# Optimization experiments

Hardware: AMD Instinct MI355X
Metric: run time of the kernel (lower is better)

## Reference

```python
import jax, jax.numpy as jnp
import numpy as np

B = 256
D = 2048          # in_channels (shared latent dim)
S = 8             # n_subjects
OUT = 1000        # sum of 7 Schaefer network head widths [150,148,132,136,76,122,236]


def setup_inputs() -> dict:
    key = jax.random.key(0)
    k1, k2, k3, k4 = jax.random.split(key, 4)
    x = jax.random.normal(k1, (B, D), dtype=jnp.float32)
    subject_ids = jax.random.randint(k2, (B,), 0, S, dtype=jnp.int64)
    scale = 1.0 / np.sqrt(D)  # matches normal_(0, 1/in_channels**0.5)
    # Concatenated per-head weights: equivalent to 7 heads of shapes
    # (S, D, n_k) concatenated along the output axis (n_k sums to OUT).
    W = jax.random.normal(k3, (S, D, OUT), dtype=jnp.float32) * scale
    b = jax.random.normal(k4, (S, OUT), dtype=jnp.float32) * scale
    return {"x": x, "subject_ids": subject_ids, "W": W, "b": b}


def reference(x, subject_ids, W, b):
    # Per-sample weight gather (B, D, OUT) followed by batched matmul,
    # exactly mirroring torch: w = weights[subject_ids]; einsum('bd,bdo->bo').
    w = W[subject_ids]                      # (B, D, OUT) gathered copy
    out = jnp.einsum('bd,bdo->bo', x, w)    # (B, OUT)
    out = out + b[subject_ids]              # per-subject bias
    return out
```

## Files before the change

### kernel.cpp

```cpp
#include <hip/hip_runtime.h>
#include <stdint.h>

#define Bn   256
#define Dn   2048
#define Sn   8
#define ON   1000

#define ROWS 64
#define OT   64
#define KC   256
#define NDC  (Dn / KC)
#define NCH  (KC / 32)
#define NIT  (KC / 32)
#define LDK  (KC + 8)

typedef short v8s __attribute__((ext_vector_type(8)));
typedef float v4f __attribute__((ext_vector_type(4)));

static __device__ __forceinline__ short f2bf(float f) {
    union { float f; uint32_t u; } v; v.f = f;
    uint32_t u = v.u;
    u += 0x7FFFu + ((u >> 16) & 1u);
    return (short)(u >> 16);
}

__global__ __launch_bounds__(256) void main_kernel(const float* __restrict__ x,
                                                   const int* __restrict__ sid,
                                                   const float* __restrict__ W,
                                                   float* __restrict__ part) {
    __shared__ unsigned short Ash[ROWS * LDK];
    __shared__ unsigned short Bsh[OT * LDK];
    __shared__ unsigned long long bmask[4];
    __shared__ int rows_l[ROWS];

    const int oc = blockIdx.x;
    const int dc = blockIdx.y;
    const int s  = blockIdx.z;
    const int o0 = oc * OT;
    const int d0 = dc * KC;
    const int t  = threadIdx.x;
    const int lane = t & 63;
    const int wave = t >> 6;

    const int mysid = sid[t];
    const bool match = (mysid == s);
    const unsigned long long m = __ballot(match);
    if (lane == 0) bmask[wave] = m;
    if (t < ROWS) rows_l[t] = -1;
    __syncthreads();
    if (match) {
        int pos = __popcll(m & ((1ull << lane) - 1ull));
        for (int w = 0; w < wave; ++w) pos += __popcll(bmask[w]);
        if (pos < ROWS) rows_l[pos] = t;
    }
    __syncthreads();

    const int arow = t >> 2;
    const int ag   = t & 3;
    const int xrow = rows_l[arow];
    const float* xp = (xrow >= 0) ? (x + (size_t)xrow * Dn + d0 + ag * 8) : x;
    const int aoff0 = arow * LDK + ag * 8;

    int og = o0 + lane; if (og > ON - 1) og = ON - 1;
    const float* wp = W + (size_t)s * Dn * ON + (size_t)(d0 + wave * 8) * ON + og;
    const int boff0 = lane * LDK + wave * 8;

    float4 fa[2][2];
    float  fb[2][8];
#pragma unroll
    for (int c = 0; c < 2; ++c) {
#pragma unroll
        for (int j = 0; j < 8; j++) fb[c][j] = wp[(size_t)(c * 32 + j) * ON];
        fa[c][0] = *(const float4*)(xp + c * 32);
        fa[c][1] = *(const float4*)(xp + c * 32 + 4);
    }

#pragma unroll
    for (int c = 0; c < NCH; ++c) {
        const int sl = c & 1;
        v8s av;
        av[0] = f2bf(fa[sl][0].x); av[1] = f2bf(fa[sl][0].y);
        av[2] = f2bf(fa[sl][0].z); av[3] = f2bf(fa[sl][0].w);
        av[4] = f2bf(fa[sl][1].x); av[5] = f2bf(fa[sl][1].y);
        av[6] = f2bf(fa[sl][1].z); av[7] = f2bf(fa[sl][1].w);
        *(v8s*)&Ash[aoff0 + c * 32] = av;

        v8s bv;
#pragma unroll
        for (int j = 0; j < 8; j++) bv[j] = f2bf(fb[sl][j]);
        *(v8s*)&Bsh[boff0 + c * 32] = bv;

        if (c + 2 < NCH) {
#pragma unroll
            for (int j = 0; j < 8; j++) fb[sl][j] = wp[(size_t)((c + 2) * 32 + j) * ON];
            fa[sl][0] = *(const float4*)(xp + (c + 2) * 32);
            fa[sl][1] = *(const float4*)(xp + (c + 2) * 32 + 4);
        }
    }

    __syncthreads();

    const int lo16 = lane & 15;
    const int quad = lane >> 4;
    const int ar   = wave * 16 + lo16;

    v4f acc[4];
#pragma unroll
    for (int i = 0; i < 4; i++) acc[i] = (v4f){0.f, 0.f, 0.f, 0.f};

#pragma unroll
    for (int it = 0; it < NIT; ++it) {
        const v8s af = *(const v8s*)&Ash[ar * LDK + it * 32 + quad * 8];
#pragma unroll
        for (int nt = 0; nt < 4; nt++) {
            const v8s bf = *(const v8s*)&Bsh[(nt * 16 + lo16) * LDK + it * 32 + quad * 8];
            acc[nt] = __builtin_amdgcn_mfma_f32_16x16x32_bf16(af, bf, acc[nt], 0, 0, 0);
        }
    }

    float* pp = part + (size_t)dc * Bn * ON;
    const int er0 = wave * 16 + quad * 4;
#pragma unroll
    for (int nt = 0; nt < 4; nt++) {
        const int o = o0 + nt * 16 + lo16;
        if (o < ON) {
#pragma unroll
            for (int r = 0; r < 4; r++) {
                const int bi = rows_l[er0 + r];
                if (bi >= 0) pp[(size_t)bi * ON + o] = acc[nt][r];
            }
        }
    }
}

__global__ __launch_bounds__(256) void reduce_kernel(const int* __restrict__ sid,
                                                     const float* __restrict__ bias,
                                                     const float* __restrict__ part,
                                                     float* __restrict__ out) {
    const int b = blockIdx.x;
    const int s = sid[b];
    const int o = threadIdx.x * 4;
    if (o < ON) {
        float4 v = *(const float4*)(bias + (size_t)s * ON + o);
#pragma unroll
        for (int d = 0; d < NDC; d++) {
            const float4 p = *(const float4*)(part + ((size_t)d * Bn + b) * ON + o);
            v.x += p.x; v.y += p.y; v.z += p.z; v.w += p.w;
        }
        *(float4*)(out + (size_t)b * ON + o) = v;
    }
}

extern "C" void kernel_launch(void* const* d_in, const int* in_sizes, int n_in,
                              void* d_out, int out_size, void* d_ws, size_t ws_size,
                              hipStream_t stream) {
    const float* x    = (const float*)d_in[0];
    const int*   sid  = (const int*)d_in[1];
    const float* W    = (const float*)d_in[2];
    const float* bias = (const float*)d_in[3];
    float*       out  = (float*)d_out;
    float*       part = (float*)d_ws;

    main_kernel<<<dim3(16, NDC, Sn), dim3(256), 0, stream>>>(x, sid, W, part);
    reduce_kernel<<<dim3(Bn), dim3(256), 0, stream>>>(sid, bias, part, out);
}
```

Measured before the change: 111.9 us.

## Fuse split-K partials and reduction into single kernel with double-buffered K loop

Drops the split-K grid and the separate reduce kernel. Each block now loops over the full D dimension with double-buffered LDS and register prefetch of the next chunks, and adds the bias directly when it writes the output. This removes the partial-sum traffic to workspace and the second launch. In exchange the grid shrinks to 256 blocks with launch_bounds(256,1) and large register arrays, so latency hiding rests on the prefetch depth and occupancy may drop.

```diff
diff --git a/kernel.cpp b/kernel.cpp
--- a/kernel.cpp
+++ b/kernel.cpp
@@ -7,12 +7,10 @@
 #define ON   1000
 
 #define ROWS 64
-#define OT   64
-#define KC   256
-#define NDC  (Dn / KC)
-#define NCH  (KC / 32)
-#define NIT  (KC / 32)
-#define LDK  (KC + 8)
+#define OT   32
+#define CK   256
+#define NCH  (Dn / CK)
+#define LDK  (CK + 8)
 
 typedef short v8s __attribute__((ext_vector_type(8)));
 typedef float v4f __attribute__((ext_vector_type(4)));
@@ -24,26 +22,24 @@
     return (short)(u >> 16);
 }
 
-__global__ __launch_bounds__(256) void main_kernel(const float* __restrict__ x,
-                                                   const int* __restrict__ sid,
-                                                   const float* __restrict__ W,
-                                                   float* __restrict__ part) {
-    __shared__ unsigned short Ash[ROWS * LDK];
-    __shared__ unsigned short Bsh[OT * LDK];
+__global__ __launch_bounds__(256, 1) void fused_kernel(const float* __restrict__ x,
+                                                       const int* __restrict__ sid,
+                                                       const float* __restrict__ W,
+                                                       const float* __restrict__ bias,
+                                                       float* __restrict__ out) {
+    __shared__ unsigned short Ash[2][ROWS * LDK];
+    __shared__ unsigned short Bsh[2][OT * LDK];
     __shared__ unsigned long long bmask[4];
     __shared__ int rows_l[ROWS];
 
     const int oc = blockIdx.x;
-    const int dc = blockIdx.y;
-    const int s  = blockIdx.z;
+    const int s  = blockIdx.y;
     const int o0 = oc * OT;
-    const int d0 = dc * KC;
     const int t  = threadIdx.x;
     const int lane = t & 63;
     const int wave = t >> 6;
 
-    const int mysid = sid[t];
-    const bool match = (mysid == s);
+    const bool match = (sid[t] == s);
     const unsigned long long m = __ballot(match);
     if (lane == 0) bmask[wave] = m;
     if (t < ROWS) rows_l[t] = -1;
@@ -58,96 +54,91 @@
     const int arow = t >> 2;
     const int ag   = t & 3;
     const int xrow = rows_l[arow];
-    const float* xp = (xrow >= 0) ? (x + (size_t)xrow * Dn + d0 + ag * 8) : x;
-    const int aoff0 = arow * LDK + ag * 8;
+    const float* xp = (xrow >= 0) ? (x + (size_t)xrow * Dn + ag * 8) : x;
+    const int aoff = arow * LDK + ag * 8;
 
-    int og = o0 + lane; if (og > ON - 1) og = ON - 1;
-    const float* wp = W + (size_t)s * Dn * ON + (size_t)(d0 + wave * 8) * ON + og;
-    const int boff0 = lane * LDK + wave * 8;
+    int og = o0 + (t & 31); if (og > ON - 1) og = ON - 1;
+    const int kg = t >> 5;
+    const float* wp = W + (size_t)s * Dn * ON + (size_t)(kg * 8) * ON + og;
+    const int boff = (t & 31) * LDK + kg * 8;
 
-    float4 fa[2][2];
-    float  fb[2][8];
-#pragma unroll
-    for (int c = 0; c < 2; ++c) {
-#pragma unroll
-        for (int j = 0; j < 8; j++) fb[c][j] = wp[(size_t)(c * 32 + j) * ON];
-        fa[c][0] = *(const float4*)(xp + c * 32);
-        fa[c][1] = *(const float4*)(xp + c * 32 + 4);
+    float4 fa[2][16];
+    float  fb[2][32];
+
+#define LOAD_CHUNK(slot, c)                                                          \
+    {                                                                                \
+        _Pragma("unroll")                                                            \
+        for (int j = 0; j < 8; j++) {                                                \
+            fa[slot][2*j]   = *(const float4*)(xp + (c) * CK + j * 32);              \
+            fa[slot][2*j+1] = *(const float4*)(xp + (c) * CK + j * 32 + 4);          \
+        }                                                                            \
+        _Pragma("unroll")                                                            \
+        for (int j = 0; j < 4; j++)                                                  \
+            _Pragma("unroll")                                                        \
+            for (int e = 0; e < 8; e++)                                              \
+                fb[slot][j*8+e] = wp[(size_t)((c) * CK + j * 64 + e) * ON];          \
     }
-
-#pragma unroll
-    for (int c = 0; c < NCH; ++c) {
-        const int sl = c & 1;
-        v8s av;
-        av[0] = f2bf(fa[sl][0].x); av[1] = f2bf(fa[sl][0].y);
-        av[2] = f2bf(fa[sl][0].z); av[3] = f2bf(fa[sl][0].w);
-        av[4] = f2bf(fa[sl][1].x); av[5] = f2bf(fa[sl][1].y);
-        av[6] = f2bf(fa[sl][1].z); av[7] = f2bf(fa[sl][1].w);
-        *(v8s*)&Ash[aoff0 + c * 32] = av;
-
-        v8s bv;
-#pragma unroll
-        for (int j = 0; j < 8; j++) bv[j] = f2bf(fb[sl][j]);
-        *(v8s*)&Bsh[boff0 + c * 32] = bv;
-
-        if (c + 2 < NCH) {
-#pragma unroll
-            for (int j = 0; j < 8; j++) fb[sl][j] = wp[(size_t)((c + 2) * 32 + j) * ON];
-            fa[sl][0] = *(const float4*)(xp + (c + 2) * 32);
-            fa[sl][1] = *(const float4*)(xp + (c + 2) * 32 + 4);
-        }
-    }
-
-    __syncthreads();
 
     const int lo16 = lane & 15;
     const int quad = lane >> 4;
-    const int ar   = wave * 16 + lo16;
+    const int ar_off = (wave * 16 + lo16) * LDK;
 
-    v4f acc[4];
+    v4f acc[2];
+    acc[0] = (v4f){0.f, 0.f, 0.f, 0.f};
+    acc[1] = (v4f){0.f, 0.f, 0.f, 0.f};
+
+    LOAD_CHUNK(0, 0)
+    LOAD_CHUNK(1, 1)
+
+    for (int c = 0; c < NCH; ++c) {
+        const int sl = c & 1;
+
+        unsigned short* Ab = &Ash[sl][0];
+        unsigned short* Bb = &Bsh[sl][0];
 #pragma unroll
-    for (int i = 0; i < 4; i++) acc[i] = (v4f){0.f, 0.f, 0.f, 0.f};
+        for (int j = 0; j < 8; j++) {
+            const float4 f0 = fa[sl][2*j], f1 = fa[sl][2*j+1];
+            v8s av;
+            av[0] = f2bf(f0.x); av[1] = f2bf(f0.y); av[2] = f2bf(f0.z); av[3] = f2bf(f0.w);
+            av[4] = f2bf(f1.x); av[5] = f2bf(f1.y); av[6] = f2bf(f1.z); av[7] = f2bf(f1.w);
+            *(v8s*)&Ab[aoff + j * 32] = av;
+        }
+#pragma unroll
+        for (int j = 0; j < 4; j++) {
+            v8s bv;
+#pragma unroll
+            for (int e = 0; e < 8; e++) bv[e] = f2bf(fb[sl][j*8+e]);
+            *(v8s*)&Bb[boff + j * 64] = bv;
+        }
+
+        __syncthreads();
+
+        if (c + 2 < NCH) LOAD_CHUNK(sl, c + 2)
 
 #pragma unroll
-    for (int it = 0; it < NIT; ++it) {
-        const v8s af = *(const v8s*)&Ash[ar * LDK + it * 32 + quad * 8];
+        for (int it = 0; it < 8; ++it) {
+            const v8s af = *(const v8s*)&Ab[ar_off + it * 32 + quad * 8];
 #pragma unroll
-        for (int nt = 0; nt < 4; nt++) {
-            const v8s bf = *(const v8s*)&Bsh[(nt * 16 + lo16) * LDK + it * 32 + quad * 8];
-            acc[nt] = __builtin_amdgcn_mfma_f32_16x16x32_bf16(af, bf, acc[nt], 0, 0, 0);
+            for (int nt = 0; nt < 2; nt++) {
+                const v8s bf = *(const v8s*)&Bb[(nt * 16 + lo16) * LDK + it * 32 + quad * 8];
+                acc[nt] = __builtin_amdgcn_mfma_f32_16x16x32_bf16(af, bf, acc[nt], 0, 0, 0);
+            }
         }
     }
+#undef LOAD_CHUNK
 
-    float* pp = part + (size_t)dc * Bn * ON;
     const int er0 = wave * 16 + quad * 4;
 #pragma unroll
-    for (int nt = 0; nt < 4; nt++) {
+    for (int nt = 0; nt < 2; nt++) {
         const int o = o0 + nt * 16 + lo16;
         if (o < ON) {
+            const float bv = bias[(size_t)s * ON + o];
 #pragma unroll
             for (int r = 0; r < 4; r++) {
                 const int bi = rows_l[er0 + r];
-                if (bi >= 0) pp[(size_t)bi * ON + o] = acc[nt][r];
+                if (bi >= 0) out[(size_t)bi * ON + o] = acc[nt][r] + bv;
             }
         }
-    }
-}
-
-__global__ __launch_bounds__(256) void reduce_kernel(const int* __restrict__ sid,
-                                                     const float* __restrict__ bias,
-                                                     const float* __restrict__ part,
-                                                     float* __restrict__ out) {
-    const int b = blockIdx.x;
-    const int s = sid[b];
-    const int o = threadIdx.x * 4;
-    if (o < ON) {
-        float4 v = *(const float4*)(bias + (size_t)s * ON + o);
-#pragma unroll
-        for (int d = 0; d < NDC; d++) {
-            const float4 p = *(const float4*)(part + ((size_t)d * Bn + b) * ON + o);
-            v.x += p.x; v.y += p.y; v.z += p.z; v.w += p.w;
-        }
-        *(float4*)(out + (size_t)b * ON + o) = v;
     }
 }
 
@@ -159,8 +150,6 @@
     const float* W    = (const float*)d_in[2];
     const float* bias = (const float*)d_in[3];
     float*       out  = (float*)d_out;
-    float*       part = (float*)d_ws;
 
-    main_kernel<<<dim3(16, NDC, Sn), dim3(256), 0, stream>>>(x, sid, W, part);
-    reduce_kernel<<<dim3(Bn), dim3(256), 0, stream>>>(sid, bias, part, out);
+    fused_kernel<<<dim3(32, Sn), dim3(256), 0, stream>>>(x, sid, W, bias, out);
 }
```

Result: slower. 179.5 us (+60.5%).

## Halve output tile, issue all global loads upfront, reorder grid for more blocks

Applied to the files above, without the earlier changes.

Output tile width drops from 64 to 32 columns, which doubles the grid to 2048 blocks; the grid is reordered so subject varies fastest. Each thread now issues all of its x and W loads at once into registers (16 float4 plus 32 scalars) rather than streaming through a two-stage register double buffer, to raise memory-level parallelism for the bandwidth-bound weight read. Launch bounds ask for 3 blocks per CU. The risks are higher register pressure and narrower 32-wide coalesced W rows, and each x row is now reloaded by twice as many blocks.

```diff
diff --git a/kernel.cpp b/kernel.cpp
--- a/kernel.cpp
+++ b/kernel.cpp
@@ -7,11 +7,9 @@
 #define ON   1000
 
 #define ROWS 64
-#define OT   64
+#define OT   32
 #define KC   256
 #define NDC  (Dn / KC)
-#define NCH  (KC / 32)
-#define NIT  (KC / 32)
 #define LDK  (KC + 8)
 
 typedef short v8s __attribute__((ext_vector_type(8)));
@@ -24,26 +22,25 @@
     return (short)(u >> 16);
 }
 
-__global__ __launch_bounds__(256) void main_kernel(const float* __restrict__ x,
-                                                   const int* __restrict__ sid,
-                                                   const float* __restrict__ W,
-                                                   float* __restrict__ part) {
+__global__ __launch_bounds__(256, 3) void main_kernel(const float* __restrict__ x,
+                                                      const int* __restrict__ sid,
+                                                      const float* __restrict__ W,
+                                                      float* __restrict__ part) {
     __shared__ unsigned short Ash[ROWS * LDK];
     __shared__ unsigned short Bsh[OT * LDK];
     __shared__ unsigned long long bmask[4];
     __shared__ int rows_l[ROWS];
 
-    const int oc = blockIdx.x;
-    const int dc = blockIdx.y;
-    const int s  = blockIdx.z;
+    const int s  = blockIdx.x;
+    const int oc = blockIdx.y;
+    const int dc = blockIdx.z;
     const int o0 = oc * OT;
     const int d0 = dc * KC;
     const int t  = threadIdx.x;
     const int lane = t & 63;
     const int wave = t >> 6;
 
-    const int mysid = sid[t];
-    const bool match = (mysid == s);
+    const bool match = (sid[t] == s);
     const unsigned long long m = __ballot(match);
     if (lane == 0) bmask[wave] = m;
     if (t < ROWS) rows_l[t] = -1;
@@ -59,60 +56,57 @@
     const int ag   = t & 3;
     const int xrow = rows_l[arow];
     const float* xp = (xrow >= 0) ? (x + (size_t)xrow * Dn + d0 + ag * 8) : x;
-    const int aoff0 = arow * LDK + ag * 8;
+    const int aoff = arow * LDK + ag * 8;
 
-    int og = o0 + lane; if (og > ON - 1) og = ON - 1;
-    const float* wp = W + (size_t)s * Dn * ON + (size_t)(d0 + wave * 8) * ON + og;
-    const int boff0 = lane * LDK + wave * 8;
+    int og = o0 + (t & 31); if (og > ON - 1) og = ON - 1;
+    const int kg = t >> 5;
+    const float* wp = W + (size_t)s * Dn * ON + (size_t)(d0 + kg * 8) * ON + og;
+    const int boff = (t & 31) * LDK + kg * 8;
 
-    float4 fa[2][2];
-    float  fb[2][8];
+    float4 a[16];
 #pragma unroll
-    for (int c = 0; c < 2; ++c) {
+    for (int j = 0; j < 8; j++) {
+        a[2*j]   = *(const float4*)(xp + j * 32);
+        a[2*j+1] = *(const float4*)(xp + j * 32 + 4);
+    }
+    float b[32];
 #pragma unroll
-        for (int j = 0; j < 8; j++) fb[c][j] = wp[(size_t)(c * 32 + j) * ON];
-        fa[c][0] = *(const float4*)(xp + c * 32);
-        fa[c][1] = *(const float4*)(xp + c * 32 + 4);
-    }
+    for (int g = 0; g < 4; g++)
+#pragma unroll
+        for (int e = 0; e < 8; e++)
+            b[g*8+e] = wp[(size_t)(g * 64 + e) * ON];
 
 #pragma unroll
-    for (int c = 0; c < NCH; ++c) {
-        const int sl = c & 1;
+    for (int j = 0; j < 8; j++) {
+        const float4 f0 = a[2*j], f1 = a[2*j+1];
         v8s av;
-        av[0] = f2bf(fa[sl][0].x); av[1] = f2bf(fa[sl][0].y);
-        av[2] = f2bf(fa[sl][0].z); av[3] = f2bf(fa[sl][0].w);
-        av[4] = f2bf(fa[sl][1].x); av[5] = f2bf(fa[sl][1].y);
-        av[6] = f2bf(fa[sl][1].z); av[7] = f2bf(fa[sl][1].w);
-        *(v8s*)&Ash[aoff0 + c * 32] = av;
-
+        av[0] = f2bf(f0.x); av[1] = f2bf(f0.y); av[2] = f2bf(f0.z); av[3] = f2bf(f0.w);
+        av[4] = f2bf(f1.x); av[5] = f2bf(f1.y); av[6] = f2bf(f1.z); av[7] = f2bf(f1.w);
+        *(v8s*)&Ash[aoff + j * 32] = av;
+    }
+#pragma unroll
+    for (int g = 0; g < 4; g++) {
         v8s bv;
 #pragma unroll
-        for (int j = 0; j < 8; j++) bv[j] = f2bf(fb[sl][j]);
-        *(v8s*)&Bsh[boff0 + c * 32] = bv;
-
-        if (c + 2 < NCH) {
-#pragma unroll
-            for (int j = 0; j < 8; j++) fb[sl][j] = wp[(size_t)((c + 2) * 32 + j) * ON];
-            fa[sl][0] = *(const float4*)(xp + (c + 2) * 32);
-            fa[sl][1] = *(const float4*)(xp + (c + 2) * 32 + 4);
-        }
+        for (int e = 0; e < 8; e++) bv[e] = f2bf(b[g*8+e]);
+        *(v8s*)&Bsh[boff + g * 64] = bv;
     }
 
     __syncthreads();
 
     const int lo16 = lane & 15;
     const int quad = lane >> 4;
-    const int ar   = wave * 16 + lo16;
+    const int ar_off = (wave * 16 + lo16) * LDK;
 
-    v4f acc[4];
-#pragma unroll
-    for (int i = 0; i < 4; i++) acc[i] = (v4f){0.f, 0.f, 0.f, 0.f};
+    v4f acc[2];
+    acc[0] = (v4f){0.f, 0.f, 0.f, 0.f};
+    acc[1] = (v4f){0.f, 0.f, 0.f, 0.f};
 
 #pragma unroll
-    for (int it = 0; it < NIT; ++it) {
-        const v8s af = *(const v8s*)&Ash[ar * LDK + it * 32 + quad * 8];
+    for (int it = 0; it < 8; ++it) {
+        const v8s af = *(const v8s*)&Ash[ar_off + it * 32 + quad * 8];
 #pragma unroll
-        for (int nt = 0; nt < 4; nt++) {
+        for (int nt = 0; nt < 2; nt++) {
             const v8s bf = *(const v8s*)&Bsh[(nt * 16 + lo16) * LDK + it * 32 + quad * 8];
             acc[nt] = __builtin_amdgcn_mfma_f32_16x16x32_bf16(af, bf, acc[nt], 0, 0, 0);
         }
@@ -121,7 +115,7 @@
     float* pp = part + (size_t)dc * Bn * ON;
     const int er0 = wave * 16 + quad * 4;
 #pragma unroll
-    for (int nt = 0; nt < 4; nt++) {
+    for (int nt = 0; nt < 2; nt++) {
         const int o = o0 + nt * 16 + lo16;
         if (o < ON) {
 #pragma unroll
@@ -161,6 +155,6 @@
     float*       out  = (float*)d_out;
     float*       part = (float*)d_ws;
 
-    main_kernel<<<dim3(16, NDC, Sn), dim3(256), 0, stream>>>(x, sid, W, part);
+    main_kernel<<<dim3(Sn, 32, NDC), dim3(256), 0, stream>>>(x, sid, W, part);
     reduce_kernel<<<dim3(Bn), dim3(256), 0, stream>>>(sid, bias, part, out);
 }
```

After: 113.5 us. About the same (+1.5%).
